# Kernel optimization log

Measured on AMD Instinct MI355X. Metric: run time of the kernel, lower is better.

Reference implementation:

```python
import jax, jax.numpy as jnp
import numpy as np

ALPHA = 2.0  # snntorch ATan surrogate default

@jax.custom_vjp
def atan_spike(x):
    return (x > 0).astype(x.dtype)

def _atan_fwd(x):
    return (x > 0).astype(x.dtype), x

def _atan_bwd(x, g):
    return (g * (ALPHA / 2.0) / (1.0 + (jnp.pi / 2.0 * ALPHA * x) ** 2),)

atan_spike.defvjp(_atan_fwd, _atan_bwd)

def leaky_step(x, mem, beta, thr):
    # snntorch Leaky, reset_mechanism='subtract': reset from PREVIOUS mem (detached)
    b = jnp.clip(beta, 0.0, 1.0)
    reset = jax.lax.stop_gradient((mem - thr > 0).astype(mem.dtype))
    mem_new = b * mem + x - reset * thr
    spk = atan_spike(mem_new - thr)
    return spk, mem_new

B, D_IN, D_H, P = 4096, 2048, 2048, 1024

def setup_inputs() -> dict:
    key = jax.random.key(0)
    ks = jax.random.split(key, 32)
    def lin_params(k, fan_in, fan_out):
        bound = 1.0 / np.sqrt(fan_in)
        kw, kb = jax.random.split(k)
        W = jax.random.uniform(kw, (fan_out, fan_in), minval=-bound, maxval=bound, dtype=jnp.float32)
        b = jax.random.uniform(kb, (fan_out,), minval=-bound, maxval=bound, dtype=jnp.float32)
        return W, b
    inp = {}
    for n, i in zip(["spk_x_1", "spk_x_2", "spk_x_3", "spk_x_4", "hidden_prev"], range(5)):
        inp[n] = (jax.random.uniform(ks[i], (B, D_IN if i < 4 else D_H)) < 0.2).astype(jnp.float32)
    inp["syn_prev"] = jax.random.normal(ks[5], (B, D_H), dtype=jnp.float32)
    inp["mem_forget"] = jax.random.normal(ks[6], (B, P), dtype=jnp.float32)
    inp["mem_input"] = jax.random.normal(ks[7], (B, P), dtype=jnp.float32)
    inp["mem_gate"] = jax.random.normal(ks[8], (B, P), dtype=jnp.float32)
    inp["mem_output"] = jax.random.normal(ks[9], (B, P), dtype=jnp.float32)
    inp["mem_hidden"] = jax.random.normal(ks[10], (B, D_H), dtype=jnp.float32)
    names = [("Wif", D_IN), ("Whf", D_H), ("Wii", D_IN), ("Whi", D_H), ("Wig", D_IN), ("Whg", D_H), ("Wio", D_IN), ("Who", D_H)]
    for j, (n, fi) in enumerate(names):
        fo = P
        W, b = lin_params(ks[11 + j], fi, fo)
        inp[n + "_w"] = W
        inp[n + "_b"] = b
    for n in ["forget", "input", "gate", "output", "hidden"]:
        inp["beta_" + n] = jnp.float32(0.9)
        inp["thr_" + n] = jnp.float32(1.0)
    return inp

def reference(spk_x_1, spk_x_2, spk_x_3, spk_x_4, hidden_prev, syn_prev,
              mem_forget, mem_input, mem_gate, mem_output, mem_hidden,
              Wif_w, Wif_b, Whf_w, Whf_b, Wii_w, Wii_b, Whi_w, Whi_b,
              Wig_w, Wig_b, Whg_w, Whg_b, Wio_w, Wio_b, Who_w, Who_b,
              beta_forget, thr_forget, beta_input, thr_input, beta_gate, thr_gate,
              beta_output, thr_output, beta_hidden, thr_hidden):
    def lin(x, W, b):
        return x @ W.T + b
    enc_f = lin(spk_x_1, Wif_w, Wif_b) + lin(hidden_prev, Whf_w, Whf_b)
    spk_f, mem_f = leaky_step(enc_f, mem_forget, beta_forget, thr_forget)
    f = jax.nn.sigmoid(jnp.mean(spk_f, axis=1, keepdims=True))  # [B,1]
    enc_i = lin(spk_x_2, Wii_w, Wii_b) + lin(hidden_prev, Whi_w, Whi_b)
    spk_i, mem_i = leaky_step(enc_i, mem_input, beta_input, thr_input)
    i = jax.nn.sigmoid(jnp.mean(spk_i, axis=1, keepdims=True))
    enc_g = lin(spk_x_3, Wig_w, Wig_b) + lin(hidden_prev, Whg_w, Whg_b)
    spk_g, mem_g = leaky_step(enc_g, mem_gate, beta_gate, thr_gate)
    g = jnp.tanh(jnp.mean(spk_g, axis=1, keepdims=True))
    enc_o = lin(spk_x_4, Wio_w, Wio_b) + lin(hidden_prev, Who_w, Who_b)
    spk_o, mem_o = leaky_step(enc_o, mem_output, beta_output, thr_output)
    o = jax.nn.sigmoid(jnp.mean(spk_o, axis=1, keepdims=True))
    syn = f * syn_prev + i * g  # [B, D_H]
    mem_h_in = o * jnp.tanh(syn)
    hidden, mem_h = leaky_step(mem_h_in, mem_hidden, beta_hidden, thr_hidden)
    return (hidden, syn, mem_f, mem_i, mem_g, mem_o, mem_h)
```

## Files before the change

### kernel.cpp

```cpp
#include <hip/hip_runtime.h>

typedef int v4i __attribute__((ext_vector_type(4)));

#define OFF_SYN   8388608ull
#define OFF_MEM   16777216ull
#define OFF_MEMH  33554432ull
#define AQ01_BYTE  50331648ull
#define AQ234_BYTE 134217728ull
#define A_BYTES    8388608ull

struct PackArgs { const int4* src[5]; int4* dst[5]; };
struct WArgs    { const float* W1[4]; const float* W2[4]; signed char* Wq; };
struct GArgs {
  const signed char* ax[4];
  const signed char* ah;
  const signed char* Wq;
  const float* mem[4];
  const float* b1[4];
  const float* b2[4];
  const float* beta[4];
  const float* thr[4];
  float* out;
};
struct CArgs {
  const float* memo; const float* syn_prev; const float* mem_hidden;
  const float* thr[4]; const float* beta_h; const float* thr_h;
  float* hid; float* syn; float* memh;
};

__device__ __forceinline__ void gload16(const void* gsrc, void* lds) {
  __builtin_amdgcn_global_load_lds(
      (__attribute__((address_space(1))) void*)(gsrc),
      (__attribute__((address_space(3))) void*)(lds), 16, 0, 0);
}

__global__ __launch_bounds__(256) void k_pack(PackArgs a) {
  unsigned idx = blockIdx.x * 256u + threadIdx.x;
  unsigned arr = idx >> 19;
  unsigned off = idx & 524287u;
  const int4* s = a.src[arr] + (size_t)off * 4;
  int4 v0 = s[0], v1 = s[1], v2 = s[2], v3 = s[3];
  union { signed char c[16]; int4 v; } u;
  u.c[0]=(signed char)(v0.x!=0); u.c[1]=(signed char)(v0.y!=0);
  u.c[2]=(signed char)(v0.z!=0); u.c[3]=(signed char)(v0.w!=0);
  u.c[4]=(signed char)(v1.x!=0); u.c[5]=(signed char)(v1.y!=0);
  u.c[6]=(signed char)(v1.z!=0); u.c[7]=(signed char)(v1.w!=0);
  u.c[8]=(signed char)(v2.x!=0); u.c[9]=(signed char)(v2.y!=0);
  u.c[10]=(signed char)(v2.z!=0); u.c[11]=(signed char)(v2.w!=0);
  u.c[12]=(signed char)(v3.x!=0); u.c[13]=(signed char)(v3.y!=0);
  u.c[14]=(signed char)(v3.z!=0); u.c[15]=(signed char)(v3.w!=0);
  a.dst[arr][off] = u.v;
}

__global__ __launch_bounds__(256) void k_wdig(WArgs a) {
  unsigned idx = blockIdx.x * 256u + threadIdx.x;
  unsigned g  = idx >> 20;
  unsigned n  = (idx >> 10) & 1023u;
  unsigned kk = (idx & 1023u) << 2;
  const float* src = (kk < 2048u) ? (a.W1[g] + (size_t)n * 2048 + kk)
                                  : (a.W2[g] + (size_t)n * 2048 + (kk - 2048u));
  float4 w = *(const float4*)src;
  float wv[4] = {w.x, w.y, w.z, w.w};
  union { signed char c[4]; int i; } u0, u1, u2;
  #pragma unroll
  for (int e = 0; e < 4; ++e) {
    long long q = llrint((double)wv[e] * 268435456.0);
    long long r0 = ((q + 128) & 255) - 128; q = (q - r0) / 256;
    long long r1 = ((q + 128) & 255) - 128; q = (q - r1) / 256;
    u0.c[e] = (signed char)r0; u1.c[e] = (signed char)r1; u2.c[e] = (signed char)q;
  }
  size_t gb = (size_t)g * 3ull * 1024ull * 4096ull;
  size_t base = (size_t)n * 4096 + kk;
  *(int*)(a.Wq + gb + 0ull * 4194304ull + base) = u0.i;
  *(int*)(a.Wq + gb + 1ull * 4194304ull + base) = u1.i;
  *(int*)(a.Wq + gb + 2ull * 4194304ull + base) = u2.i;
}

__global__ __launch_bounds__(256, 2) void k_gemm(GArgs a) {
  __shared__ __align__(16) signed char As[2][128 * 128];
  __shared__ __align__(16) signed char Bs[2][3][64 * 128];
  const int tid = threadIdx.x;
  const int w = tid >> 6, l = tid & 63;
  const int wr = w >> 1, wc = w & 1;
  const int g = blockIdx.z, mt = blockIdx.y, nt = blockIdx.x;
  const int lr = l >> 3;
  const int lk = l & 7;

  v4i acc[3][4][2];
  v4i zero = {0, 0, 0, 0};
  #pragma unroll
  for (int d = 0; d < 3; ++d)
    #pragma unroll
    for (int mi = 0; mi < 4; ++mi)
      #pragma unroll
      for (int ni = 0; ni < 2; ++ni) acc[d][mi][ni] = zero;

  const signed char* Wg = a.Wq + (size_t)g * 3ull * 4194304ull
                               + (size_t)(nt * 64) * 4096ull;

  auto stage = [&](int buf, int K0) {
    const signed char* Ab; int kl;
    if (K0 < 2048) { Ab = a.ax[g]; kl = K0; } else { Ab = a.ah; kl = K0 - 2048; }
    #pragma unroll
    for (int c = 0; c < 4; ++c) {
      int s = w * 4 + c;
      int rl = s * 8 + lr;
      gload16(Ab + (size_t)(mt * 128 + rl) * 2048 + kl + ((lk ^ (rl & 7)) << 4),
              &As[buf][s * 1024]);
    }
    #pragma unroll
    for (int c = 0; c < 6; ++c) {
      int idx = c * 4 + w;
      int d = idx >> 3, seg = idx & 7;
      int rl = seg * 8 + lr;
      gload16(Wg + (size_t)d * 4194304ull + (size_t)rl * 4096ull + K0
                 + ((lk ^ (rl & 7)) << 4),
              &Bs[buf][d][seg * 1024]);
    }
  };

  stage(0, 0);
  int cur = 0;
  for (int t = 0; t < 32; ++t) {
    __syncthreads();

    v4i av[2][4];
    v4i bv[2][3][2];
    #pragma unroll
    for (int h = 0; h < 2; ++h) {
      #pragma unroll
      for (int mi = 0; mi < 4; ++mi) {
        int ar = wr * 64 + mi * 16 + (l & 15);
        int cp = ((h << 2) + (l >> 4)) ^ (ar & 7);
        av[h][mi] = *(const v4i*)&As[cur][ar * 128 + cp * 16];
      }
      #pragma unroll
      for (int d = 0; d < 3; ++d)
        #pragma unroll
        for (int ni = 0; ni < 2; ++ni) {
          int br = wc * 32 + ni * 16 + (l & 15);
          int cp = ((h << 2) + (l >> 4)) ^ (br & 7);
          bv[h][d][ni] = *(const v4i*)&Bs[cur][d][br * 128 + cp * 16];
        }
    }
    if (t + 1 < 32) stage(cur ^ 1, (t + 1) * 128);
    __builtin_amdgcn_sched_barrier(0);

    __builtin_amdgcn_s_setprio(1);
    #pragma unroll
    for (int h = 0; h < 2; ++h)
      #pragma unroll
      for (int d = 0; d < 3; ++d)
        #pragma unroll
        for (int mi = 0; mi < 4; ++mi)
          #pragma unroll
          for (int ni = 0; ni < 2; ++ni)
            acc[d][mi][ni] = __builtin_amdgcn_mfma_i32_16x16x64_i8(
                av[h][mi], bv[h][d][ni], acc[d][mi][ni], 0, 0, 0);
    __builtin_amdgcn_s_setprio(0);
    __builtin_amdgcn_sched_barrier(0);
    cur ^= 1;
  }

  const float* b1 = a.b1[g];
  const float* b2 = a.b2[g];
  const float* memg = a.mem[g];
  float* outg = a.out + (size_t)g * 4194304ull;
  double beta = fmin(fmax((double)(*a.beta[g]), 0.0), 1.0);
  double thr = (double)(*a.thr[g]);
  #pragma unroll
  for (int mi = 0; mi < 4; ++mi)
    #pragma unroll
    for (int ni = 0; ni < 2; ++ni) {
      int m0 = mt * 128 + wr * 64 + mi * 16 + ((l >> 4) << 2);
      int n  = nt * 64 + wc * 32 + ni * 16 + (l & 15);
      double bsum = (double)b1[n] + (double)b2[n];
      #pragma unroll
      for (int j = 0; j < 4; ++j) {
        double e = (double)acc[2][mi][ni][j] * 65536.0
                 + (double)acc[1][mi][ni][j] * 256.0
                 + (double)acc[0][mi][ni][j];
        double enc = e * (1.0 / 268435456.0) + bsum;
        size_t o = (size_t)(m0 + j) * 1024 + n;
        double mp = (double)memg[o];
        double reset = (mp - thr > 0.0) ? 1.0 : 0.0;
        double mn = beta * mp + enc - reset * thr;
        outg[o] = (float)mn;
      }
    }
}

__global__ __launch_bounds__(256) void k_fin(CArgs a) {
  const int b = blockIdx.x, tid = threadIdx.x;
  const int w = tid >> 6, l = tid & 63;
  __shared__ int scnt[4];
  __shared__ double sval[3];
  const float* mg = a.memo + (size_t)w * 4194304ull + (size_t)b * 1024;
  const float thrw = *a.thr[w];
  int cnt = 0;
  #pragma unroll
  for (int p = 0; p < 16; ++p) {
    float v = mg[l + p * 64];
    cnt += ((v - thrw) > 0.0f) ? 1 : 0;
  }
  #pragma unroll
  for (int off = 32; off; off >>= 1) cnt += __shfl_down(cnt, off, 64);
  if (l == 0) scnt[w] = cnt;
  __syncthreads();
  if (tid == 0) {
    double mf = scnt[0] * (1.0 / 1024.0);
    double mi = scnt[1] * (1.0 / 1024.0);
    double mgv = scnt[2] * (1.0 / 1024.0);
    double mo = scnt[3] * (1.0 / 1024.0);
    double f  = 1.0 / (1.0 + exp(-mf));
    double ii = 1.0 / (1.0 + exp(-mi));
    double gv = tanh(mgv);
    double oo = 1.0 / (1.0 + exp(-mo));
    sval[0] = f; sval[1] = ii * gv; sval[2] = oo;
  }
  __syncthreads();
  const double f = sval[0], ig = sval[1], oo = sval[2];
  const double bh = fmin(fmax((double)(*a.beta_h), 0.0), 1.0);
  const double th = (double)(*a.thr_h);
  const size_t rb = (size_t)b * 2048;
  for (int j = tid; j < 2048; j += 256) {
    double s = f * (double)a.syn_prev[rb + j] + ig;
    double mp = (double)a.mem_hidden[rb + j];
    double reset = (mp - th > 0.0) ? 1.0 : 0.0;
    double mh = bh * mp + oo * tanh(s) - reset * th;
    a.syn[rb + j] = (float)s;
    a.memh[rb + j] = (float)mh;
    a.hid[rb + j] = ((mh - th) > 0.0) ? 1.0f : 0.0f;
  }
}

extern "C" void kernel_launch(void* const* d_in, const int* in_sizes, int n_in,
                              void* d_out, int out_size, void* d_ws, size_t ws_size,
                              hipStream_t stream) {
  (void)in_sizes; (void)n_in; (void)out_size; (void)d_ws; (void)ws_size;
  float* out = (float*)d_out;
  signed char* base8 = (signed char*)d_out;

  PackArgs pa;
  for (int i = 0; i < 5; ++i) {
    pa.src[i] = (const int4*)d_in[i];
    pa.dst[i] = (int4*)(base8 + (i < 2 ? (AQ01_BYTE + (size_t)i * A_BYTES)
                                       : (AQ234_BYTE + (size_t)(i - 2) * A_BYTES)));
  }
  WArgs wa; wa.Wq = base8;
  for (int g = 0; g < 4; ++g) {
    wa.W1[g] = (const float*)d_in[11 + 4 * g];
    wa.W2[g] = (const float*)d_in[13 + 4 * g];
  }
  GArgs ga;
  for (int g = 0; g < 4; ++g) {
    ga.ax[g]   = (const signed char*)pa.dst[g];
    ga.mem[g]  = (const float*)d_in[6 + g];
    ga.b1[g]   = (const float*)d_in[12 + 4 * g];
    ga.b2[g]   = (const float*)d_in[14 + 4 * g];
    ga.beta[g] = (const float*)d_in[27 + 2 * g];
    ga.thr[g]  = (const float*)d_in[28 + 2 * g];
  }
  ga.ah = (const signed char*)pa.dst[4];
  ga.Wq = base8;
  ga.out = out + OFF_MEM;

  CArgs ca;
  ca.memo = out + OFF_MEM;
  ca.syn_prev = (const float*)d_in[5];
  ca.mem_hidden = (const float*)d_in[10];
  for (int g = 0; g < 4; ++g) ca.thr[g] = (const float*)d_in[28 + 2 * g];
  ca.beta_h = (const float*)d_in[35];
  ca.thr_h = (const float*)d_in[36];
  ca.hid = out;
  ca.syn = out + OFF_SYN;
  ca.memh = out + OFF_MEMH;

  k_pack<<<10240, 256, 0, stream>>>(pa);
  k_wdig<<<16384, 256, 0, stream>>>(wa);
  k_gemm<<<dim3(16, 32, 4), 256, 0, stream>>>(ga);
  k_fin<<<4096, 256, 0, stream>>>(ca);
}
```

Measured before the change: 317.5 us.

## Load A operand directly from global into registers, bypassing LDS

The A tile is no longer staged through shared memory. Each wave loads its MFMA A fragments straight from global memory into double-buffered registers (avA/avB), one step ahead, while B keeps its LDS double buffer. The loop is unrolled by two so the register buffers swap without copies. This removes LDS writes, reads and footprint for A, at the cost of more VGPRs and less coalesced 16-byte global loads, since the two waves sharing a row block now fetch the same A data separately.

```diff
diff --git a/kernel.cpp b/kernel.cpp
--- a/kernel.cpp
+++ b/kernel.cpp
@@ -77,14 +77,11 @@
 }
 
 __global__ __launch_bounds__(256, 2) void k_gemm(GArgs a) {
-  __shared__ __align__(16) signed char As[2][128 * 128];
   __shared__ __align__(16) signed char Bs[2][3][64 * 128];
   const int tid = threadIdx.x;
   const int w = tid >> 6, l = tid & 63;
   const int wr = w >> 1, wc = w & 1;
   const int g = blockIdx.z, mt = blockIdx.y, nt = blockIdx.x;
-  const int lr = l >> 3;
-  const int lk = l & 7;
 
   v4i acc[3][4][2];
   v4i zero = {0, 0, 0, 0};
@@ -98,42 +95,41 @@
   const signed char* Wg = a.Wq + (size_t)g * 3ull * 4194304ull
                                + (size_t)(nt * 64) * 4096ull;
 
-  auto stage = [&](int buf, int K0) {
+  v4i avA[2][4], avB[2][4];
+  auto loadA = [&](v4i (&dst)[2][4], int t) {
+    int K0 = t * 128;
     const signed char* Ab; int kl;
     if (K0 < 2048) { Ab = a.ax[g]; kl = K0; } else { Ab = a.ah; kl = K0 - 2048; }
-    #pragma unroll
-    for (int c = 0; c < 4; ++c) {
-      int s = w * 4 + c;
-      int rl = s * 8 + lr;
-      gload16(Ab + (size_t)(mt * 128 + rl) * 2048 + kl + ((lk ^ (rl & 7)) << 4),
-              &As[buf][s * 1024]);
-    }
-    #pragma unroll
-    for (int c = 0; c < 6; ++c) {
-      int idx = c * 4 + w;
-      int d = idx >> 3, seg = idx & 7;
-      int rl = seg * 8 + lr;
-      gload16(Wg + (size_t)d * 4194304ull + (size_t)rl * 4096ull + K0
-                 + ((lk ^ (rl & 7)) << 4),
-              &Bs[buf][d][seg * 1024]);
+    const signed char* base = Ab
+        + (size_t)(mt * 128 + wr * 64 + (l & 15)) * 2048
+        + kl + ((l >> 4) << 4);
+    #pragma unroll
+    for (int h = 0; h < 2; ++h)
+      #pragma unroll
+      for (int mi = 0; mi < 4; ++mi)
+        dst[h][mi] = *(const v4i*)(base + mi * 16 * 2048 + h * 64);
+  };
+
+  auto stageB = [&](int buf, int t) {
+    int K0 = t * 128;
+    #pragma unroll
+    for (int i = 0; i < 6; ++i) {
+      int seg = i * 4 + w;
+      int d = seg >> 3, rb = (seg & 7) * 8;
+      int row = rb + (l >> 3);
+      int cg = (l & 7) ^ (row & 7);
+      gload16(Wg + (size_t)d * 4194304ull + (size_t)row * 4096ull + K0
+                 + (cg << 4),
+              &Bs[buf][d][rb * 128]);
     }
   };
 
-  stage(0, 0);
-  int cur = 0;
-  for (int t = 0; t < 32; ++t) {
+  auto step = [&](v4i (&avU)[2][4], v4i (&avL)[2][4], int t, bool pf) {
     __syncthreads();
-
-    v4i av[2][4];
+    const int cur = t & 1;
     v4i bv[2][3][2];
     #pragma unroll
-    for (int h = 0; h < 2; ++h) {
-      #pragma unroll
-      for (int mi = 0; mi < 4; ++mi) {
-        int ar = wr * 64 + mi * 16 + (l & 15);
-        int cp = ((h << 2) + (l >> 4)) ^ (ar & 7);
-        av[h][mi] = *(const v4i*)&As[cur][ar * 128 + cp * 16];
-      }
+    for (int h = 0; h < 2; ++h)
       #pragma unroll
       for (int d = 0; d < 3; ++d)
         #pragma unroll
@@ -142,10 +138,8 @@
           int cp = ((h << 2) + (l >> 4)) ^ (br & 7);
           bv[h][d][ni] = *(const v4i*)&Bs[cur][d][br * 128 + cp * 16];
         }
-    }
-    if (t + 1 < 32) stage(cur ^ 1, (t + 1) * 128);
+    if (pf) { loadA(avL, t + 1); stageB(cur ^ 1, t + 1); }
     __builtin_amdgcn_sched_barrier(0);
-
     __builtin_amdgcn_s_setprio(1);
     #pragma unroll
     for (int h = 0; h < 2; ++h)
@@ -156,11 +150,19 @@
           #pragma unroll
           for (int ni = 0; ni < 2; ++ni)
             acc[d][mi][ni] = __builtin_amdgcn_mfma_i32_16x16x64_i8(
-                av[h][mi], bv[h][d][ni], acc[d][mi][ni], 0, 0, 0);
+                avU[h][mi], bv[h][d][ni], acc[d][mi][ni], 0, 0, 0);
     __builtin_amdgcn_s_setprio(0);
     __builtin_amdgcn_sched_barrier(0);
-    cur ^= 1;
-  }
+  };
+
+  loadA(avA, 0);
+  stageB(0, 0);
+  for (int tt = 0; tt < 15; ++tt) {
+    step(avA, avB, 2 * tt, true);
+    step(avB, avA, 2 * tt + 1, true);
+  }
+  step(avA, avB, 30, true);
+  step(avB, avA, 31, false);
 
   const float* b1 = a.b1[g];
   const float* b2 = a.b2[g];
```

After: 461.6 us. 1.45x slower.

## Fuse spike counting into GEMM epilogue and use 32-bit weight digit split

Applied to the files above, without the earlier changes.

The GEMM epilogue now takes a wave ballot of which new membrane values exceed the threshold. It writes per-row partial spike counts to the workspace. The final kernel reads these small partial counts instead of re-reading all four 4096x1024 membrane outputs to count spikes, which removes a large global-memory read pass. Separately, the weight quantization kernel switches from double/64-bit integer math to float/32-bit integer math for splitting weights into int8 digits. The GEMM writes counts through the workspace pointer unconditionally, even though the finalize kernel only uses them when a large enough workspace is provided.

```diff
diff --git a/kernel.cpp b/kernel.cpp
--- a/kernel.cpp
+++ b/kernel.cpp
@@ -8,6 +8,7 @@
 #define AQ01_BYTE  50331648ull
 #define AQ234_BYTE 134217728ull
 #define A_BYTES    8388608ull
+#define CNT_BYTES  2097152ull
 
 struct PackArgs { const int4* src[5]; int4* dst[5]; };
 struct WArgs    { const float* W1[4]; const float* W2[4]; signed char* Wq; };
@@ -21,11 +22,13 @@
   const float* beta[4];
   const float* thr[4];
   float* out;
+  unsigned int* cnt;
 };
 struct CArgs {
   const float* memo; const float* syn_prev; const float* mem_hidden;
   const float* thr[4]; const float* beta_h; const float* thr_h;
   float* hid; float* syn; float* memh;
+  const unsigned int* cnt;
 };
 
 __device__ __forceinline__ void gload16(const void* gsrc, void* lds) {
@@ -64,9 +67,9 @@
   union { signed char c[4]; int i; } u0, u1, u2;
   #pragma unroll
   for (int e = 0; e < 4; ++e) {
-    long long q = llrint((double)wv[e] * 268435456.0);
-    long long r0 = ((q + 128) & 255) - 128; q = (q - r0) / 256;
-    long long r1 = ((q + 128) & 255) - 128; q = (q - r1) / 256;
+    int q = (int)lrintf(wv[e] * 268435456.0f);
+    int r0 = ((q + 128) & 255) - 128; q = (q - r0) >> 8;
+    int r1 = ((q + 128) & 255) - 128; q = (q - r1) >> 8;
     u0.c[e] = (signed char)r0; u1.c[e] = (signed char)r1; u2.c[e] = (signed char)q;
   }
   size_t gb = (size_t)g * 3ull * 1024ull * 4096ull;
@@ -168,8 +171,10 @@
   float* outg = a.out + (size_t)g * 4194304ull;
   double beta = fmin(fmax((double)(*a.beta[g]), 0.0), 1.0);
   double thr = (double)(*a.thr[g]);
+  const float thrf = *a.thr[g];
   #pragma unroll
-  for (int mi = 0; mi < 4; ++mi)
+  for (int mi = 0; mi < 4; ++mi) {
+    unsigned long long msk[2][4];
     #pragma unroll
     for (int ni = 0; ni < 2; ++ni) {
       int m0 = mt * 128 + wr * 64 + mi * 16 + ((l >> 4) << 2);
@@ -185,28 +190,52 @@
         double mp = (double)memg[o];
         double reset = (mp - thr > 0.0) ? 1.0 : 0.0;
         double mn = beta * mp + enc - reset * thr;
-        outg[o] = (float)mn;
+        float v = (float)mn;
+        outg[o] = v;
+        msk[ni][j] = __ballot(v > thrf);
       }
     }
-}
-
+    int r = l & 15, grp = r >> 2, j = r & 3;
+    unsigned c = (unsigned)__popcll((msk[0][j] >> (grp * 16)) & 0xFFFFull)
+               + (unsigned)__popcll((msk[1][j] >> (grp * 16)) & 0xFFFFull);
+    if (l < 16)
+      a.cnt[((size_t)g * 4096 + mt * 128 + wr * 64 + mi * 16 + r) * 32
+            + nt * 2 + wc] = c;
+  }
+}
+
+template <bool USE_WS>
 __global__ __launch_bounds__(256) void k_fin(CArgs a) {
   const int b = blockIdx.x, tid = threadIdx.x;
   const int w = tid >> 6, l = tid & 63;
   __shared__ int scnt[4];
   __shared__ double sval[3];
-  const float* mg = a.memo + (size_t)w * 4194304ull + (size_t)b * 1024;
-  const float thrw = *a.thr[w];
-  int cnt = 0;
-  #pragma unroll
-  for (int p = 0; p < 16; ++p) {
-    float v = mg[l + p * 64];
-    cnt += ((v - thrw) > 0.0f) ? 1 : 0;
-  }
-  #pragma unroll
-  for (int off = 32; off; off >>= 1) cnt += __shfl_down(cnt, off, 64);
-  if (l == 0) scnt[w] = cnt;
-  __syncthreads();
+  if (USE_WS) {
+    __shared__ int part[128];
+    if (tid < 128)
+      part[tid] = (int)a.cnt[((size_t)(tid >> 5) * 4096 + b) * 32 + (tid & 31)];
+    __syncthreads();
+    if (tid < 4) {
+      int s = 0;
+      #pragma unroll
+      for (int i = 0; i < 32; ++i) s += part[tid * 32 + i];
+      scnt[tid] = s;
+    }
+    __syncthreads();
+  } else {
+    const float* mg = a.memo + (size_t)w * 4194304ull + (size_t)b * 1024;
+    const float thrw = *a.thr[w];
+    int cnt = 0;
+    #pragma unroll
+    for (int p = 0; p < 16; ++p) {
+      float v = mg[l + p * 64];
+      cnt += ((v - thrw) > 0.0f) ? 1 : 0;
+    }
+    #pragma unroll
+    for (int off = 32; off; off >>= 1) cnt += __shfl_down(cnt, off, 64);
+    if (l == 0) scnt[w] = cnt;
+    __syncthreads();
+  }
   if (tid == 0) {
     double mf = scnt[0] * (1.0 / 1024.0);
     double mi = scnt[1] * (1.0 / 1024.0);
@@ -237,9 +266,10 @@
 extern "C" void kernel_launch(void* const* d_in, const int* in_sizes, int n_in,
                               void* d_out, int out_size, void* d_ws, size_t ws_size,
                               hipStream_t stream) {
-  (void)in_sizes; (void)n_in; (void)out_size; (void)d_ws; (void)ws_size;
+  (void)in_sizes; (void)n_in; (void)out_size;
   float* out = (float*)d_out;
   signed char* base8 = (signed char*)d_out;
+  const bool use_ws = (d_ws != nullptr) && (ws_size >= CNT_BYTES);
 
   PackArgs pa;
   for (int i = 0; i < 5; ++i) {
@@ -264,6 +294,7 @@
   ga.ah = (const signed char*)pa.dst[4];
   ga.Wq = base8;
   ga.out = out + OFF_MEM;
+  ga.cnt = (unsigned int*)d_ws;
 
   CArgs ca;
   ca.memo = out + OFF_MEM;
@@ -275,9 +306,11 @@
   ca.hid = out;
   ca.syn = out + OFF_SYN;
   ca.memh = out + OFF_MEMH;
+  ca.cnt = (const unsigned int*)d_ws;
 
   k_pack<<<10240, 256, 0, stream>>>(pa);
   k_wdig<<<16384, 256, 0, stream>>>(wa);
   k_gemm<<<dim3(16, 32, 4), 256, 0, stream>>>(ga);
-  k_fin<<<4096, 256, 0, stream>>>(ca);
-}
+  if (use_ws) k_fin<true><<<4096, 256, 0, stream>>>(ca);
+  else        k_fin<false><<<4096, 256, 0, stream>>>(ca);
+}
```

Measured after the change: 312.5 us. About the same (-1.6%).
